# Optimization experiments

Measured on AMD Instinct MI355X. Metric: run time of the kernel, lower is better.

The kernel has to match this reference:

```python
import jax, jax.numpy as jnp
import numpy as np

B, S, D, H = 4, 1024, 1024, 16
HD = D // H
EPS = 1e-5


def setup_inputs() -> dict:
    key = jax.random.key(0)
    ks = jax.random.split(key, 12)
    sc = 0.02
    return {
        "x": jax.random.normal(ks[0], (B, S, D), jnp.float32),
        "WQ": jax.random.normal(ks[1], (D, D), jnp.float32) * sc,
        "WK": jax.random.normal(ks[2], (D, D), jnp.float32) * sc,
        "WV": jax.random.normal(ks[3], (D, D), jnp.float32) * sc,
        "Wo": jax.random.normal(ks[4], (D, D), jnp.float32) * sc,
        "bo": jnp.zeros((D,), jnp.float32),
        "W1": jax.random.normal(ks[5], (D, 4 * D), jnp.float32) * sc,
        "b1": jnp.zeros((4 * D,), jnp.float32),
        "W2": jax.random.normal(ks[6], (4 * D, D), jnp.float32) * sc,
        "b2": jnp.zeros((D,), jnp.float32),
        "ln1_s": jnp.ones((D,), jnp.float32),
        "ln1_b": jnp.zeros((D,), jnp.float32),
        "ln2_s": jnp.ones((D,), jnp.float32),
        "ln2_b": jnp.zeros((D,), jnp.float32),
    }


def _layernorm(x, scale, shift):
    mean = jnp.mean(x, axis=-1, keepdims=True)
    var = jnp.mean((x - mean) ** 2, axis=-1, keepdims=True)  # unbiased=False
    return scale * ((x - mean) / jnp.sqrt(var + EPS)) + shift


def _gelu(x):
    c = jnp.sqrt(2.0 / jnp.pi).astype(x.dtype)
    return 0.5 * x * (1.0 + jnp.tanh(c * (x + 0.044715 * x ** 3)))


def reference(x, WQ, WK, WV, Wo, bo, W1, b1, W2, b2, ln1_s, ln1_b, ln2_s, ln2_b):
    b, s, d = x.shape
    # --- attention sub-block (pre-norm) ---
    h = _layernorm(x, ln1_s, ln1_b)
    q = (h @ WQ).reshape(b, s, H, HD).transpose(0, 2, 1, 3)  # [B,H,S,HD]
    k = (h @ WK).reshape(b, s, H, HD).transpose(0, 2, 1, 3)
    v = (h @ WV).reshape(b, s, H, HD).transpose(0, 2, 1, 3)
    scores = jnp.einsum("bhqd,bhkd->bhqk", q, k)
    causal = jnp.triu(jnp.ones((s, s), dtype=bool), k=1)
    scores = jnp.where(causal, -jnp.inf, scores)
    attn = jax.nn.softmax(scores / jnp.sqrt(jnp.float32(HD)), axis=-1)
    ctx = jnp.einsum("bhqk,bhkd->bhqd", attn, v)
    ctx = ctx.transpose(0, 2, 1, 3).reshape(b, s, d)
    x = x + (ctx @ Wo + bo)
    # --- FF sub-block (pre-norm) ---
    h = _layernorm(x, ln2_s, ln2_b)
    h = _gelu(h @ W1 + b1)
    return x + (h @ W2 + b2)
```

## Files before the change

kernel.cpp:

```cpp
#include <hip/hip_runtime.h>
#include <hip/hip_bf16.h>

#define DIM   1024
#define NHEAD 16
#define HDIM  64
#define BATCH 4
#define SEQ   1024
#define MTOT  (BATCH*SEQ)
#define DFF   (4*DIM)
#define LDQ   3072

typedef _Float16 f16x8 __attribute__((ext_vector_type(8)));
typedef _Float16 f16x4 __attribute__((ext_vector_type(4)));
typedef float    f32x4 __attribute__((ext_vector_type(4)));

__device__ __forceinline__ float geluf(float x) {
    float z2 = 1.5957691216057308f * (x + 0.044715f * x * x * x);
    return x * __builtin_amdgcn_rcpf(1.0f + __expf(-z2));
}

__device__ __forceinline__ int swz_off(int row, int slot) {
    return row * 128 + ((slot ^ (row & 7)) << 4);
}
__device__ __forceinline__ f16x8 ldsfrag(const _Float16* s, int row, int slot) {
    return *(const f16x8*)((const char*)s + swz_off(row, slot));
}

template <int NCHUNK>
__device__ __forceinline__ void stage_async(const _Float16* __restrict__ g, int ld,
                                            _Float16* s, int w, int lane) {
    int r_in = lane >> 3;
    int sslot = lane & 7;
    int lslot = sslot ^ r_in;
#pragma unroll
    for (int q = 0; q < NCHUNK; ++q) {
        int chunk = w * NCHUNK + q;
        int row = chunk * 8 + r_in;
        const _Float16* gp = g + (size_t)row * ld + lslot * 8;
        _Float16* sp = s + chunk * 512;
        __builtin_amdgcn_global_load_lds(
            (const __attribute__((address_space(1))) void*)gp,
            (__attribute__((address_space(3))) void*)sp, 16, 0, 0);
    }
}

__global__ __launch_bounds__(256) void k_tcvt(const float* __restrict__ src,
                                              _Float16* __restrict__ dst,
                                              int K, int N) {
    __shared__ float tile[32][33];
    int n0 = blockIdx.x * 32, k0 = blockIdx.y * 32;
    int tx = threadIdx.x, ty = threadIdx.y;
#pragma unroll
    for (int i = 0; i < 32; i += 8)
        tile[ty + i][tx] = src[(size_t)(k0 + ty + i) * N + (n0 + tx)];
    __syncthreads();
#pragma unroll
    for (int i = 0; i < 32; i += 8)
        dst[(size_t)(n0 + ty + i) * K + (k0 + tx)] = (_Float16)tile[tx][ty + i];
}

__global__ __launch_bounds__(256) void k_tcvt3(const float* __restrict__ s0,
                                               const float* __restrict__ s1,
                                               const float* __restrict__ s2,
                                               _Float16* __restrict__ dst) {
    __shared__ float tile[32][33];
    const float* src = blockIdx.z == 0 ? s0 : (blockIdx.z == 1 ? s1 : s2);
    _Float16* d = dst + (size_t)blockIdx.z * (1024 * 1024);
    int n0 = blockIdx.x * 32, k0 = blockIdx.y * 32;
    int tx = threadIdx.x, ty = threadIdx.y;
#pragma unroll
    for (int i = 0; i < 32; i += 8)
        tile[ty + i][tx] = src[(size_t)(k0 + ty + i) * 1024 + (n0 + tx)];
    __syncthreads();
#pragma unroll
    for (int i = 0; i < 32; i += 8)
        d[(size_t)(n0 + ty + i) * 1024 + (k0 + tx)] = (_Float16)tile[tx][ty + i];
}

__global__ __launch_bounds__(256) void k_ln(const float* __restrict__ x,
                                            const float* __restrict__ sc,
                                            const float* __restrict__ sh,
                                            _Float16* __restrict__ out) {
    int row = blockIdx.x;
    int t = threadIdx.x;
    float4 v = ((const float4*)(x + (size_t)row * DIM))[t];
    float sum = v.x + v.y + v.z + v.w;
    float sq  = v.x * v.x + v.y * v.y + v.z * v.z + v.w * v.w;
#pragma unroll
    for (int m = 1; m < 64; m <<= 1) {
        sum += __shfl_xor(sum, m);
        sq  += __shfl_xor(sq, m);
    }
    __shared__ float rs[4], rq[4];
    int w = t >> 6;
    if ((t & 63) == 0) { rs[w] = sum; rq[w] = sq; }
    __syncthreads();
    sum = rs[0] + rs[1] + rs[2] + rs[3];
    sq  = rq[0] + rq[1] + rq[2] + rq[3];
    float mean = sum * (1.0f / DIM);
    float var  = sq * (1.0f / DIM) - mean * mean;
    float rstd = rsqrtf(var + 1e-5f);
    float4 s4 = ((const float4*)sc)[t];
    float4 b4 = ((const float4*)sh)[t];
    f16x4 o;
    o[0] = (_Float16)(s4.x * ((v.x - mean) * rstd) + b4.x);
    o[1] = (_Float16)(s4.y * ((v.y - mean) * rstd) + b4.y);
    o[2] = (_Float16)(s4.z * ((v.z - mean) * rstd) + b4.z);
    o[3] = (_Float16)(s4.w * ((v.w - mean) * rstd) + b4.w);
    ((f16x4*)(out + (size_t)row * DIM))[t] = o;
}

template <int EPI>
__global__ __launch_bounds__(256) void k_gemm(const _Float16* __restrict__ A,
                                              const _Float16* __restrict__ BT,
                                              int N, int K, int gx,
                                              _Float16* __restrict__ Ch,
                                              const float* __restrict__ bias) {
    __shared__ _Float16 As[2][128 * 64];
    __shared__ _Float16 Bs[2][128 * 64];
    int t = threadIdx.x;
    int bid = blockIdx.x;
    int lin = (bid & 7) * ((int)gridDim.x >> 3) + (bid >> 3);
    int m0 = (lin / gx) * 128, n0 = (lin % gx) * 128;
    int lane = t & 63, w = t >> 6;
    int wm = (w >> 1) * 64, wn = (w & 1) * 64;
    int lr = lane & 15, lg = lane >> 4;
    f32x4 acc[4][4];
#pragma unroll
    for (int i = 0; i < 4; ++i)
#pragma unroll
        for (int j = 0; j < 4; ++j) acc[i][j] = (f32x4){0.f, 0.f, 0.f, 0.f};

    const _Float16* Ag = A  + (size_t)m0 * K;
    const _Float16* Bg = BT + (size_t)n0 * K;
    int nt = K / 64;
    stage_async<4>(Ag, K, As[0], w, lane);
    stage_async<4>(Bg, K, Bs[0], w, lane);
    __syncthreads();
    for (int tt = 0; tt < nt; ++tt) {
        int cur = tt & 1, nxt = cur ^ 1;
        if (tt + 1 < nt) {
            stage_async<4>(Ag + (tt + 1) * 64, K, As[nxt], w, lane);
            stage_async<4>(Bg + (tt + 1) * 64, K, Bs[nxt], w, lane);
        }
#pragma unroll
        for (int kk = 0; kk < 2; ++kk) {
            f16x8 a[4], b[4];
#pragma unroll
            for (int i = 0; i < 4; ++i) a[i] = ldsfrag(As[cur], wm + i * 16 + lr, kk * 4 + lg);
#pragma unroll
            for (int j = 0; j < 4; ++j) b[j] = ldsfrag(Bs[cur], wn + j * 16 + lr, kk * 4 + lg);
            __builtin_amdgcn_s_setprio(1);
#pragma unroll
            for (int i = 0; i < 4; ++i)
#pragma unroll
                for (int j = 0; j < 4; ++j)
                    acc[i][j] = __builtin_amdgcn_mfma_f32_16x16x32_f16(a[i], b[j], acc[i][j], 0, 0, 0);
            __builtin_amdgcn_s_setprio(0);
        }
        __syncthreads();
    }
#pragma unroll
    for (int i = 0; i < 4; ++i) {
#pragma unroll
        for (int j = 0; j < 4; ++j) {
            int row = m0 + wm + i * 16 + lg * 4;
            int col = n0 + wn + j * 16 + lr;
#pragma unroll
            for (int r = 0; r < 4; ++r) {
                float v = acc[i][j][r];
                size_t idx = (size_t)(row + r) * N + col;
                if constexpr (EPI == 0) Ch[idx] = (_Float16)v;
                else                    Ch[idx] = (_Float16)geluf(v + bias[col]);
            }
        }
    }
}

__global__ __launch_bounds__(256) void k_gemm64(const _Float16* __restrict__ A,
                                                const _Float16* __restrict__ BT,
                                                int N, int K,
                                                float* __restrict__ Cf,
                                                const float* __restrict__ bias,
                                                const float* __restrict__ resid) {
    __shared__ _Float16 As[3][128 * 64];
    __shared__ _Float16 Bs[3][64 * 64];
    int t = threadIdx.x;
    int bid = blockIdx.x;
    int lin = (bid & 7) * ((int)gridDim.x >> 3) + (bid >> 3);
    int gx = N / 64;
    int m0 = (lin / gx) * 128, n0 = (lin % gx) * 64;
    int lane = t & 63, w = t >> 6;
    int wm = w * 32;
    int lr = lane & 15, lg = lane >> 4;
    f32x4 acc[2][4];
#pragma unroll
    for (int i = 0; i < 2; ++i)
#pragma unroll
        for (int j = 0; j < 4; ++j) acc[i][j] = (f32x4){0.f, 0.f, 0.f, 0.f};

    const _Float16* Ag = A  + (size_t)m0 * K;
    const _Float16* Bg = BT + (size_t)n0 * K;
    int nt = K / 64;
    stage_async<4>(Ag, K, As[0], w, lane);
    stage_async<2>(Bg, K, Bs[0], w, lane);
    stage_async<4>(Ag + 64, K, As[1], w, lane);
    stage_async<2>(Bg + 64, K, Bs[1], w, lane);
    for (int tt = 0; tt < nt; ++tt) {
        if (tt + 1 < nt) asm volatile("s_waitcnt vmcnt(6)" ::: "memory");
        else             asm volatile("s_waitcnt vmcnt(0)" ::: "memory");
        __builtin_amdgcn_sched_barrier(0);
        __builtin_amdgcn_s_barrier();
        __builtin_amdgcn_sched_barrier(0);
        const _Float16* Ac = As[tt % 3];
        const _Float16* Bc = Bs[tt % 3];
#pragma unroll
        for (int kk = 0; kk < 2; ++kk) {
            f16x8 a[2], b[4];
#pragma unroll
            for (int i = 0; i < 2; ++i) a[i] = ldsfrag(Ac, wm + i * 16 + lr, kk * 4 + lg);
#pragma unroll
            for (int j = 0; j < 4; ++j) b[j] = ldsfrag(Bc, j * 16 + lr, kk * 4 + lg);
            __builtin_amdgcn_s_setprio(1);
#pragma unroll
            for (int i = 0; i < 2; ++i)
#pragma unroll
                for (int j = 0; j < 4; ++j)
                    acc[i][j] = __builtin_amdgcn_mfma_f32_16x16x32_f16(a[i], b[j], acc[i][j], 0, 0, 0);
            __builtin_amdgcn_s_setprio(0);
        }
        if (tt + 2 < nt) {
            int nb = (tt + 2) % 3;
            stage_async<4>(Ag + (tt + 2) * 64, K, As[nb], w, lane);
            stage_async<2>(Bg + (tt + 2) * 64, K, Bs[nb], w, lane);
        }
    }
#pragma unroll
    for (int i = 0; i < 2; ++i) {
#pragma unroll
        for (int j = 0; j < 4; ++j) {
            int row = m0 + wm + i * 16 + lg * 4;
            int col = n0 + j * 16 + lr;
#pragma unroll
            for (int r = 0; r < 4; ++r) {
                size_t idx = (size_t)(row + r) * N + col;
                Cf[idx] = acc[i][j][r] + bias[col] + resid[idx];
            }
        }
    }
}

__global__ __launch_bounds__(64) void k_attn(const _Float16* __restrict__ QKV,
                                             _Float16* __restrict__ Og) {
    __shared__ _Float16 Ps[32 * 64];
    int lane = threadIdx.x;
    int id = blockIdx.x;
    int bh = id & 63;
    int qt = (SEQ / 32 - 1) - (id >> 6);
    int h = bh & 15, b = bh >> 4;
    int q0 = qt * 32;
    int lr = lane & 15, lg = lane >> 4;
    size_t base = (size_t)b * SEQ;
    int cq = h * HDIM, ck = 1024 + h * HDIM, cv = 2048 + h * HDIM;

    f16x8 aq[2][2];
#pragma unroll
    for (int i = 0; i < 2; ++i)
#pragma unroll
        for (int kk = 0; kk < 2; ++kk) {
            f16x8 v = *(const f16x8*)(QKV + (base + q0 + i * 16 + lr) * LDQ + cq + kk * 32 + lg * 8);
#pragma unroll
            for (int e = 0; e < 8; ++e) v[e] = v[e] * (_Float16)0.125f;
            aq[i][kk] = v;
        }

    f32x4 cacc[2][4];
#pragma unroll
    for (int i = 0; i < 2; ++i)
#pragma unroll
        for (int j = 0; j < 4; ++j) cacc[i][j] = (f32x4){0.f, 0.f, 0.f, 0.f};
    float mrun[2][4], lrun[2][4];
#pragma unroll
    for (int i = 0; i < 2; ++i)
#pragma unroll
        for (int r = 0; r < 4; ++r) { mrun[i][r] = -1e30f; lrun[i][r] = 0.f; }

    int ntiles = q0 / 64 + 1;
    for (int kt = 0; kt < ntiles; ++kt) {
        int k0 = kt * 64;
        f32x4 sacc[2][4];
#pragma unroll
        for (int i = 0; i < 2; ++i)
#pragma unroll
            for (int j = 0; j < 4; ++j) sacc[i][j] = (f32x4){0.f, 0.f, 0.f, 0.f};
#pragma unroll
        for (int kk = 0; kk < 2; ++kk) {
            f16x8 bk[4];
#pragma unroll
            for (int j = 0; j < 4; ++j)
                bk[j] = *(const f16x8*)(QKV + (base + k0 + j * 16 + lr) * LDQ + ck + kk * 32 + lg * 8);
            __builtin_amdgcn_s_setprio(1);
#pragma unroll
            for (int i = 0; i < 2; ++i)
#pragma unroll
                for (int j = 0; j < 4; ++j)
                    sacc[i][j] = __builtin_amdgcn_mfma_f32_16x16x32_f16(aq[i][kk], bk[j], sacc[i][j], 0, 0, 0);
            __builtin_amdgcn_s_setprio(0);
        }
        if (kt == ntiles - 1) {
#pragma unroll
            for (int i = 0; i < 2; ++i)
#pragma unroll
                for (int j = 0; j < 4; ++j)
#pragma unroll
                    for (int r = 0; r < 4; ++r) {
                        int qq = q0 + i * 16 + lg * 4 + r;
                        int kc = k0 + j * 16 + lr;
                        if (kc > qq) sacc[i][j][r] = -1e30f;
                    }
        }
#pragma unroll
        for (int i = 0; i < 2; ++i) {
            float mn[4], al[4];
#pragma unroll
            for (int r = 0; r < 4; ++r) {
                float tm = fmaxf(fmaxf(sacc[i][0][r], sacc[i][1][r]),
                                 fmaxf(sacc[i][2][r], sacc[i][3][r]));
#pragma unroll
                for (int msk = 1; msk < 16; msk <<= 1) tm = fmaxf(tm, __shfl_xor(tm, msk));
                float m2 = fmaxf(mrun[i][r], tm);
                al[r] = __expf(mrun[i][r] - m2);
                mrun[i][r] = m2;
                mn[r] = m2;
            }
#pragma unroll
            for (int jd = 0; jd < 4; ++jd)
#pragma unroll
                for (int r = 0; r < 4; ++r) cacc[i][jd][r] *= al[r];
#pragma unroll
            for (int r = 0; r < 4; ++r) {
                float ps = 0.f;
#pragma unroll
                for (int j = 0; j < 4; ++j) {
                    float p = __expf(sacc[i][j][r] - mn[r]);
                    sacc[i][j][r] = p;
                    ps += p;
                }
#pragma unroll
                for (int msk = 1; msk < 16; msk <<= 1) ps += __shfl_xor(ps, msk);
                lrun[i][r] = lrun[i][r] * al[r] + ps;
            }
        }
#pragma unroll
        for (int i = 0; i < 2; ++i)
#pragma unroll
            for (int j = 0; j < 4; ++j) {
                int kc = j * 16 + lr;
                int ks = kc >> 3;
                int kb = (kc & 7) * 2;
#pragma unroll
                for (int r = 0; r < 4; ++r) {
                    int qq = i * 16 + lg * 4 + r;
                    *(_Float16*)((char*)Ps + qq * 128 + ((ks ^ (qq & 7)) << 4) + kb) =
                        (_Float16)sacc[i][j][r];
                }
            }
        {
            const _Float16* vb = QKV + (base + k0) * LDQ + cv;
#pragma unroll
            for (int kk = 0; kk < 2; ++kk) {
                f16x8 pa[2], bv[4];
#pragma unroll
                for (int i = 0; i < 2; ++i) pa[i] = ldsfrag(Ps, i * 16 + lr, kk * 4 + lg);
                const _Float16* vk = vb + (size_t)(kk * 32 + lg * 8) * LDQ + lr;
#pragma unroll
                for (int jd = 0; jd < 4; ++jd)
#pragma unroll
                    for (int e = 0; e < 8; ++e)
                        bv[jd][e] = vk[(size_t)e * LDQ + jd * 16];
                __builtin_amdgcn_s_setprio(1);
#pragma unroll
                for (int i = 0; i < 2; ++i)
#pragma unroll
                    for (int jd = 0; jd < 4; ++jd)
                        cacc[i][jd] = __builtin_amdgcn_mfma_f32_16x16x32_f16(pa[i], bv[jd], cacc[i][jd], 0, 0, 0);
                __builtin_amdgcn_s_setprio(0);
            }
        }
    }
#pragma unroll
    for (int i = 0; i < 2; ++i)
#pragma unroll
        for (int jd = 0; jd < 4; ++jd)
#pragma unroll
            for (int r = 0; r < 4; ++r) {
                int qq = q0 + i * 16 + lg * 4 + r;
                int d = h * HDIM + jd * 16 + lr;
                Og[(base + qq) * DIM + d] = (_Float16)(cacc[i][jd][r] / lrun[i][r]);
            }
}

extern "C" void kernel_launch(void* const* d_in, const int* in_sizes, int n_in,
                              void* d_out, int out_size, void* d_ws, size_t ws_size,
                              hipStream_t stream) {
    const float* x    = (const float*)d_in[0];
    const float* WQ   = (const float*)d_in[1];
    const float* WK   = (const float*)d_in[2];
    const float* WV   = (const float*)d_in[3];
    const float* Wo   = (const float*)d_in[4];
    const float* bo   = (const float*)d_in[5];
    const float* W1   = (const float*)d_in[6];
    const float* b1   = (const float*)d_in[7];
    const float* W2   = (const float*)d_in[8];
    const float* b2   = (const float*)d_in[9];
    const float* ln1s = (const float*)d_in[10];
    const float* ln1b = (const float*)d_in[11];
    const float* ln2s = (const float*)d_in[12];
    const float* ln2b = (const float*)d_in[13];
    float* out = (float*)d_out;
    char* ws = (char*)d_ws;
    const size_t MB = 1024 * 1024;
    _Float16* WTqkv = (_Float16*)(ws + 0 * MB);
    _Float16* WTo   = (_Float16*)(ws + 6 * MB);
    _Float16* WT1   = (_Float16*)(ws + 8 * MB);
    _Float16* WT2   = (_Float16*)(ws + 16 * MB);
    _Float16* h1    = (_Float16*)(ws + 24 * MB);
    _Float16* qkvb  = (_Float16*)(ws + 32 * MB);
    _Float16* ctx   = (_Float16*)(ws + 56 * MB);
    _Float16* h2    = (_Float16*)(ws + 64 * MB);
    _Float16* ff1   = (_Float16*)(ws + 72 * MB);
    float*    x2    = (float*)   (ws + 104 * MB);

    dim3 tb(32, 8);
    k_tcvt3<<<dim3(32, 32, 3), tb, 0, stream>>>(WQ, WK, WV, WTqkv);
    k_tcvt<<<dim3(32, 32), tb, 0, stream>>>(Wo, WTo, 1024, 1024);
    k_tcvt<<<dim3(128, 32), tb, 0, stream>>>(W1, WT1, 1024, 4096);
    k_tcvt<<<dim3(32, 128), tb, 0, stream>>>(W2, WT2, 4096, 1024);

    k_ln<<<MTOT, 256, 0, stream>>>(x, ln1s, ln1b, h1);

    k_gemm<0><<<dim3(768), 256, 0, stream>>>(h1, WTqkv, LDQ, DIM, 24, qkvb, nullptr);

    k_attn<<<dim3(2048), 64, 0, stream>>>(qkvb, ctx);

    k_gemm64<<<dim3(512), 256, 0, stream>>>(ctx, WTo, DIM, DIM, x2, bo, x);

    k_ln<<<MTOT, 256, 0, stream>>>(x2, ln2s, ln2b, h2);

    k_gemm<1><<<dim3(1024), 256, 0, stream>>>(h2, WT1, DFF, DIM, 32, ff1, b1);

    k_gemm64<<<dim3(512), 256, 0, stream>>>(ff1, WT2, DIM, DFF, out, b2, x2);
}
```

Baseline: 235.1 us.

## Split attention into 16-row query tiles with four independent waves per block

The attention kernel now gives each wave a 16-row query tile instead of 32 rows, and packs four waves per 256-thread block, each with its own LDS probability buffer. This doubles the number of waves, lowers register pressure per wave and spreads the causal workload more finely, to improve occupancy and latency hiding. The trade-off is that K and V tiles are reloaded from global memory twice as often per query row.

```diff
diff --git a/kernel.cpp b/kernel.cpp
--- a/kernel.cpp
+++ b/kernel.cpp
@@ -250,49 +250,43 @@
     }
 }
 
-__global__ __launch_bounds__(64) void k_attn(const _Float16* __restrict__ QKV,
-                                             _Float16* __restrict__ Og) {
-    __shared__ _Float16 Ps[32 * 64];
-    int lane = threadIdx.x;
-    int id = blockIdx.x;
+__global__ __launch_bounds__(256) void k_attn(const _Float16* __restrict__ QKV,
+                                              _Float16* __restrict__ Og) {
+    __shared__ _Float16 PsA[4][16 * 64];
+    int t = threadIdx.x;
+    int lane = t & 63, w = t >> 6;
+    int id = blockIdx.x * 4 + w;
     int bh = id & 63;
-    int qt = (SEQ / 32 - 1) - (id >> 6);
+    int qt = 63 - (id >> 6);
     int h = bh & 15, b = bh >> 4;
-    int q0 = qt * 32;
+    int q0 = qt * 16;
     int lr = lane & 15, lg = lane >> 4;
     size_t base = (size_t)b * SEQ;
     int cq = h * HDIM, ck = 1024 + h * HDIM, cv = 2048 + h * HDIM;
-
-    f16x8 aq[2][2];
-#pragma unroll
-    for (int i = 0; i < 2; ++i)
-#pragma unroll
-        for (int kk = 0; kk < 2; ++kk) {
-            f16x8 v = *(const f16x8*)(QKV + (base + q0 + i * 16 + lr) * LDQ + cq + kk * 32 + lg * 8);
-#pragma unroll
-            for (int e = 0; e < 8; ++e) v[e] = v[e] * (_Float16)0.125f;
-            aq[i][kk] = v;
-        }
-
-    f32x4 cacc[2][4];
-#pragma unroll
-    for (int i = 0; i < 2; ++i)
-#pragma unroll
-        for (int j = 0; j < 4; ++j) cacc[i][j] = (f32x4){0.f, 0.f, 0.f, 0.f};
-    float mrun[2][4], lrun[2][4];
-#pragma unroll
-    for (int i = 0; i < 2; ++i)
-#pragma unroll
-        for (int r = 0; r < 4; ++r) { mrun[i][r] = -1e30f; lrun[i][r] = 0.f; }
+    _Float16* Ps = &PsA[w][0];
+
+    f16x8 aq[2];
+#pragma unroll
+    for (int kk = 0; kk < 2; ++kk) {
+        f16x8 v = *(const f16x8*)(QKV + (base + q0 + lr) * LDQ + cq + kk * 32 + lg * 8);
+#pragma unroll
+        for (int e = 0; e < 8; ++e) v[e] = v[e] * (_Float16)0.125f;
+        aq[kk] = v;
+    }
+
+    f32x4 cacc[4];
+#pragma unroll
+    for (int j = 0; j < 4; ++j) cacc[j] = (f32x4){0.f, 0.f, 0.f, 0.f};
+    float mrun[4], lrun[4];
+#pragma unroll
+    for (int r = 0; r < 4; ++r) { mrun[r] = -1e30f; lrun[r] = 0.f; }
 
     int ntiles = q0 / 64 + 1;
     for (int kt = 0; kt < ntiles; ++kt) {
         int k0 = kt * 64;
-        f32x4 sacc[2][4];
-#pragma unroll
-        for (int i = 0; i < 2; ++i)
-#pragma unroll
-            for (int j = 0; j < 4; ++j) sacc[i][j] = (f32x4){0.f, 0.f, 0.f, 0.f};
+        f32x4 sacc[4];
+#pragma unroll
+        for (int j = 0; j < 4; ++j) sacc[j] = (f32x4){0.f, 0.f, 0.f, 0.f};
 #pragma unroll
         for (int kk = 0; kk < 2; ++kk) {
             f16x8 bk[4];
@@ -301,77 +295,69 @@
                 bk[j] = *(const f16x8*)(QKV + (base + k0 + j * 16 + lr) * LDQ + ck + kk * 32 + lg * 8);
             __builtin_amdgcn_s_setprio(1);
 #pragma unroll
-            for (int i = 0; i < 2; ++i)
-#pragma unroll
-                for (int j = 0; j < 4; ++j)
-                    sacc[i][j] = __builtin_amdgcn_mfma_f32_16x16x32_f16(aq[i][kk], bk[j], sacc[i][j], 0, 0, 0);
+            for (int j = 0; j < 4; ++j)
+                sacc[j] = __builtin_amdgcn_mfma_f32_16x16x32_f16(aq[kk], bk[j], sacc[j], 0, 0, 0);
             __builtin_amdgcn_s_setprio(0);
         }
         if (kt == ntiles - 1) {
 #pragma unroll
-            for (int i = 0; i < 2; ++i)
-#pragma unroll
-                for (int j = 0; j < 4; ++j)
-#pragma unroll
-                    for (int r = 0; r < 4; ++r) {
-                        int qq = q0 + i * 16 + lg * 4 + r;
-                        int kc = k0 + j * 16 + lr;
-                        if (kc > qq) sacc[i][j][r] = -1e30f;
-                    }
-        }
-#pragma unroll
-        for (int i = 0; i < 2; ++i) {
+            for (int j = 0; j < 4; ++j)
+#pragma unroll
+                for (int r = 0; r < 4; ++r) {
+                    int qq = q0 + lg * 4 + r;
+                    int kc = k0 + j * 16 + lr;
+                    if (kc > qq) sacc[j][r] = -1e30f;
+                }
+        }
+        {
             float mn[4], al[4];
 #pragma unroll
             for (int r = 0; r < 4; ++r) {
-                float tm = fmaxf(fmaxf(sacc[i][0][r], sacc[i][1][r]),
-                                 fmaxf(sacc[i][2][r], sacc[i][3][r]));
+                float tm = fmaxf(fmaxf(sacc[0][r], sacc[1][r]),
+                                 fmaxf(sacc[2][r], sacc[3][r]));
 #pragma unroll
                 for (int msk = 1; msk < 16; msk <<= 1) tm = fmaxf(tm, __shfl_xor(tm, msk));
-                float m2 = fmaxf(mrun[i][r], tm);
-                al[r] = __expf(mrun[i][r] - m2);
-                mrun[i][r] = m2;
+                float m2 = fmaxf(mrun[r], tm);
+                al[r] = __expf(mrun[r] - m2);
+                mrun[r] = m2;
                 mn[r] = m2;
             }
 #pragma unroll
             for (int jd = 0; jd < 4; ++jd)
 #pragma unroll
-                for (int r = 0; r < 4; ++r) cacc[i][jd][r] *= al[r];
+                for (int r = 0; r < 4; ++r) cacc[jd][r] *= al[r];
 #pragma unroll
             for (int r = 0; r < 4; ++r) {
                 float ps = 0.f;
 #pragma unroll
                 for (int j = 0; j < 4; ++j) {
-                    float p = __expf(sacc[i][j][r] - mn[r]);
-                    sacc[i][j][r] = p;
+                    float p = __expf(sacc[j][r] - mn[r]);
+                    sacc[j][r] = p;
                     ps += p;
                 }
 #pragma unroll
                 for (int msk = 1; msk < 16; msk <<= 1) ps += __shfl_xor(ps, msk);
-                lrun[i][r] = lrun[i][r] * al[r] + ps;
-            }
-        }
-#pragma unroll
-        for (int i = 0; i < 2; ++i)
-#pragma unroll
-            for (int j = 0; j < 4; ++j) {
-                int kc = j * 16 + lr;
-                int ks = kc >> 3;
-                int kb = (kc & 7) * 2;
-#pragma unroll
-                for (int r = 0; r < 4; ++r) {
-                    int qq = i * 16 + lg * 4 + r;
-                    *(_Float16*)((char*)Ps + qq * 128 + ((ks ^ (qq & 7)) << 4) + kb) =
-                        (_Float16)sacc[i][j][r];
-                }
-            }
+                lrun[r] = lrun[r] * al[r] + ps;
+            }
+        }
+#pragma unroll
+        for (int j = 0; j < 4; ++j) {
+            int kc = j * 16 + lr;
+            int ks = kc >> 3;
+            int kb = (kc & 7) * 2;
+#pragma unroll
+            for (int r = 0; r < 4; ++r) {
+                int qq = lg * 4 + r;
+                *(_Float16*)((char*)Ps + qq * 128 + ((ks ^ (qq & 7)) << 4) + kb) =
+                    (_Float16)sacc[j][r];
+            }
+        }
         {
             const _Float16* vb = QKV + (base + k0) * LDQ + cv;
 #pragma unroll
             for (int kk = 0; kk < 2; ++kk) {
-                f16x8 pa[2], bv[4];
-#pragma unroll
-                for (int i = 0; i < 2; ++i) pa[i] = ldsfrag(Ps, i * 16 + lr, kk * 4 + lg);
+                f16x8 pa, bv[4];
+                pa = ldsfrag(Ps, lr, kk * 4 + lg);
                 const _Float16* vk = vb + (size_t)(kk * 32 + lg * 8) * LDQ + lr;
 #pragma unroll
                 for (int jd = 0; jd < 4; ++jd)
@@ -380,24 +366,20 @@
                         bv[jd][e] = vk[(size_t)e * LDQ + jd * 16];
                 __builtin_amdgcn_s_setprio(1);
 #pragma unroll
-                for (int i = 0; i < 2; ++i)
-#pragma unroll
-                    for (int jd = 0; jd < 4; ++jd)
-                        cacc[i][jd] = __builtin_amdgcn_mfma_f32_16x16x32_f16(pa[i], bv[jd], cacc[i][jd], 0, 0, 0);
+                for (int jd = 0; jd < 4; ++jd)
+                    cacc[jd] = __builtin_amdgcn_mfma_f32_16x16x32_f16(pa, bv[jd], cacc[jd], 0, 0, 0);
                 __builtin_amdgcn_s_setprio(0);
             }
         }
     }
 #pragma unroll
-    for (int i = 0; i < 2; ++i)
-#pragma unroll
-        for (int jd = 0; jd < 4; ++jd)
-#pragma unroll
-            for (int r = 0; r < 4; ++r) {
-                int qq = q0 + i * 16 + lg * 4 + r;
-                int d = h * HDIM + jd * 16 + lr;
-                Og[(base + qq) * DIM + d] = (_Float16)(cacc[i][jd][r] / lrun[i][r]);
-            }
+    for (int jd = 0; jd < 4; ++jd)
+#pragma unroll
+        for (int r = 0; r < 4; ++r) {
+            int qq = q0 + lg * 4 + r;
+            int d = h * HDIM + jd * 16 + lr;
+            Og[(base + qq) * DIM + d] = (_Float16)(cacc[jd][r] / lrun[r]);
+        }
 }
 
 extern "C" void kernel_launch(void* const* d_in, const int* in_sizes, int n_in,
@@ -441,7 +423,7 @@
 
     k_gemm<0><<<dim3(768), 256, 0, stream>>>(h1, WTqkv, LDQ, DIM, 24, qkvb, nullptr);
 
-    k_attn<<<dim3(2048), 64, 0, stream>>>(qkvb, ctx);
+    k_attn<<<dim3(1024), 256, 0, stream>>>(qkvb, ctx);
 
     k_gemm64<<<dim3(512), 256, 0, stream>>>(ctx, WTo, DIM, DIM, x2, bo, x);
 
```

Result: no change. 233.9 us (-0.5%).

## Swap MFMA operands so each lane owns a query row in attention softmax

Applied to the files above, without the earlier changes.

Swaps the A/B operands of the QK^T and PV MFMAs, so the accumulator is laid out transposed and each lane holds a single query row with four consecutive key/dim columns. Softmax row max and sum become mostly in-register reductions needing only two cross-lane shuffles instead of four per element row, and the running max/sum state shrinks from 8 to 2 scalars per lane. P tile writes to LDS and the output stores become 4-wide f16 vector stores instead of scalar half stores. The causal mask and the LDS/global indexing are rewritten to match the new layout, which carries a correctness risk if any index is off.

```diff
diff --git a/kernel.cpp b/kernel.cpp
--- a/kernel.cpp
+++ b/kernel.cpp
@@ -279,11 +279,9 @@
     for (int i = 0; i < 2; ++i)
 #pragma unroll
         for (int j = 0; j < 4; ++j) cacc[i][j] = (f32x4){0.f, 0.f, 0.f, 0.f};
-    float mrun[2][4], lrun[2][4];
-#pragma unroll
-    for (int i = 0; i < 2; ++i)
-#pragma unroll
-        for (int r = 0; r < 4; ++r) { mrun[i][r] = -1e30f; lrun[i][r] = 0.f; }
+    float mrun[2], lrun[2];
+#pragma unroll
+    for (int i = 0; i < 2; ++i) { mrun[i] = -1e30f; lrun[i] = 0.f; }
 
     int ntiles = q0 / 64 + 1;
     for (int kt = 0; kt < ntiles; ++kt) {
@@ -304,67 +302,64 @@
             for (int i = 0; i < 2; ++i)
 #pragma unroll
                 for (int j = 0; j < 4; ++j)
-                    sacc[i][j] = __builtin_amdgcn_mfma_f32_16x16x32_f16(aq[i][kk], bk[j], sacc[i][j], 0, 0, 0);
+                    sacc[i][j] = __builtin_amdgcn_mfma_f32_16x16x32_f16(bk[j], aq[i][kk], sacc[i][j], 0, 0, 0);
             __builtin_amdgcn_s_setprio(0);
         }
         if (kt == ntiles - 1) {
 #pragma unroll
-            for (int i = 0; i < 2; ++i)
+            for (int i = 0; i < 2; ++i) {
+                int qq = q0 + i * 16 + lr;
 #pragma unroll
                 for (int j = 0; j < 4; ++j)
 #pragma unroll
                     for (int r = 0; r < 4; ++r) {
-                        int qq = q0 + i * 16 + lg * 4 + r;
-                        int kc = k0 + j * 16 + lr;
+                        int kc = k0 + j * 16 + lg * 4 + r;
                         if (kc > qq) sacc[i][j][r] = -1e30f;
                     }
+            }
         }
 #pragma unroll
         for (int i = 0; i < 2; ++i) {
-            float mn[4], al[4];
-#pragma unroll
-            for (int r = 0; r < 4; ++r) {
-                float tm = fmaxf(fmaxf(sacc[i][0][r], sacc[i][1][r]),
-                                 fmaxf(sacc[i][2][r], sacc[i][3][r]));
-#pragma unroll
-                for (int msk = 1; msk < 16; msk <<= 1) tm = fmaxf(tm, __shfl_xor(tm, msk));
-                float m2 = fmaxf(mrun[i][r], tm);
-                al[r] = __expf(mrun[i][r] - m2);
-                mrun[i][r] = m2;
-                mn[r] = m2;
-            }
+            float tm = -1e30f;
+#pragma unroll
+            for (int j = 0; j < 4; ++j)
+#pragma unroll
+                for (int r = 0; r < 4; ++r) tm = fmaxf(tm, sacc[i][j][r]);
+            tm = fmaxf(tm, __shfl_xor(tm, 16));
+            tm = fmaxf(tm, __shfl_xor(tm, 32));
+            float m2 = fmaxf(mrun[i], tm);
+            float al = __expf(mrun[i] - m2);
+            mrun[i] = m2;
 #pragma unroll
             for (int jd = 0; jd < 4; ++jd)
 #pragma unroll
-                for (int r = 0; r < 4; ++r) cacc[i][jd][r] *= al[r];
-#pragma unroll
-            for (int r = 0; r < 4; ++r) {
-                float ps = 0.f;
-#pragma unroll
-                for (int j = 0; j < 4; ++j) {
-                    float p = __expf(sacc[i][j][r] - mn[r]);
+                for (int r = 0; r < 4; ++r) cacc[i][jd][r] *= al;
+            float ps = 0.f;
+#pragma unroll
+            for (int j = 0; j < 4; ++j)
+#pragma unroll
+                for (int r = 0; r < 4; ++r) {
+                    float p = __expf(sacc[i][j][r] - m2);
                     sacc[i][j][r] = p;
                     ps += p;
                 }
-#pragma unroll
-                for (int msk = 1; msk < 16; msk <<= 1) ps += __shfl_xor(ps, msk);
-                lrun[i][r] = lrun[i][r] * al[r] + ps;
+            ps += __shfl_xor(ps, 16);
+            ps += __shfl_xor(ps, 32);
+            lrun[i] = lrun[i] * al + ps;
+        }
+#pragma unroll
+        for (int i = 0; i < 2; ++i) {
+            int q = i * 16 + lr;
+#pragma unroll
+            for (int j = 0; j < 4; ++j) {
+                int kc0 = j * 16 + lg * 4;
+                int ks = kc0 >> 3;
+                f16x4 pv4;
+#pragma unroll
+                for (int r = 0; r < 4; ++r) pv4[r] = (_Float16)sacc[i][j][r];
+                *(f16x4*)((char*)Ps + q * 128 + ((ks ^ (q & 7)) << 4) + (kc0 & 7) * 2) = pv4;
             }
         }
-#pragma unroll
-        for (int i = 0; i < 2; ++i)
-#pragma unroll
-            for (int j = 0; j < 4; ++j) {
-                int kc = j * 16 + lr;
-                int ks = kc >> 3;
-                int kb = (kc & 7) * 2;
-#pragma unroll
-                for (int r = 0; r < 4; ++r) {
-                    int qq = i * 16 + lg * 4 + r;
-                    *(_Float16*)((char*)Ps + qq * 128 + ((ks ^ (qq & 7)) << 4) + kb) =
-                        (_Float16)sacc[i][j][r];
-                }
-            }
         {
             const _Float16* vb = QKV + (base + k0) * LDQ + cv;
 #pragma unroll
@@ -383,21 +378,23 @@
                 for (int i = 0; i < 2; ++i)
 #pragma unroll
                     for (int jd = 0; jd < 4; ++jd)
-                        cacc[i][jd] = __builtin_amdgcn_mfma_f32_16x16x32_f16(pa[i], bv[jd], cacc[i][jd], 0, 0, 0);
+                        cacc[i][jd] = __builtin_amdgcn_mfma_f32_16x16x32_f16(bv[jd], pa[i], cacc[i][jd], 0, 0, 0);
                 __builtin_amdgcn_s_setprio(0);
             }
         }
     }
 #pragma unroll
-    for (int i = 0; i < 2; ++i)
-#pragma unroll
-        for (int jd = 0; jd < 4; ++jd)
-#pragma unroll
-            for (int r = 0; r < 4; ++r) {
-                int qq = q0 + i * 16 + lg * 4 + r;
-                int d = h * HDIM + jd * 16 + lr;
-                Og[(base + qq) * DIM + d] = (_Float16)(cacc[i][jd][r] / lrun[i][r]);
-            }
+    for (int i = 0; i < 2; ++i) {
+        float rl = 1.0f / lrun[i];
+        int qq = q0 + i * 16 + lr;
+#pragma unroll
+        for (int jd = 0; jd < 4; ++jd) {
+            f16x4 o4;
+#pragma unroll
+            for (int r = 0; r < 4; ++r) o4[r] = (_Float16)(cacc[i][jd][r] * rl);
+            *(f16x4*)(Og + (base + qq) * DIM + h * HDIM + jd * 16 + lg * 4) = o4;
+        }
+    }
 }
 
 extern "C" void kernel_launch(void* const* d_in, const int* in_sizes, int n_in,
```

New measurement: 225.8 us. 4.0% less time.
